# Optimization experiments

Hardware: AMD Instinct MI355X
Metric: run time of the kernel (lower is better)

The kernel has to match this reference:

```python
import jax, jax.numpy as jnp
import numpy as np


def setup_inputs() -> dict:
    key = jax.random.key(0)
    k1, = jax.random.split(key, 1)
    b, l, h, w, c = 2, 16, 16, 16, 32
    inputs = jax.random.normal(k1, (b, l, h, w, c), dtype=jnp.float32)
    gamma = jnp.ones((1,), dtype=jnp.float32)
    return {"inputs": inputs, "gamma": gamma}


def reference(inputs, gamma):
    b, l, h, w, c = inputs.shape
    n = l * h * w
    # torch: x = permute->view gives [b, c, n]; here keep [b, n, c] (same memory layout of values)
    xr = inputs.reshape(b, n, c)
    # scores[b,i,j] = sum_c x[b,c,i] * x[b,c,j]
    scores = jnp.einsum('bic,bjc->bij', xr, xr)
    attn = jax.nn.softmax(scores, axis=-1)  # softmax over j (dim=-1)
    # out[b,c,j] = sum_i x[b,c,i] * attn[b,i,j]  ->  [b, n, c] layout
    out = jnp.einsum('bic,bij->bjc', xr, attn)
    out = out.reshape(b, l, h, w, c)
    return out * gamma + inputs
```

## Files before the change

### kernel.cpp

```cpp
#include <hip/hip_runtime.h>


typedef _Float16 half8 __attribute__((ext_vector_type(8)));
typedef _Float16 half4v __attribute__((ext_vector_type(4)));
typedef float float4v __attribute__((ext_vector_type(4)));

#define NN 4096
#define CC 32
#define L2E 1.44269504f
#define SHIFT 48.0f

__global__ __launch_bounds__(256) void k_convert(const float* __restrict__ x,
                                                 _Float16* __restrict__ xf,
                                                 _Float16* __restrict__ xt) {
    const int t = blockIdx.x * 256 + threadIdx.x;
    const int n  = t & 4095;
    const int cg = (t >> 12) & 7;
    const int b  = t >> 15;
    const int row = (b << 12) | n;
    const float4* src = (const float4*)(x + (size_t)row * CC + cg * 4);
    float4 v = *src;
    _Float16 h0 = (_Float16)v.x, h1 = (_Float16)v.y, h2 = (_Float16)v.z, h3 = (_Float16)v.w;
    *(half4v*)(xf + (size_t)row * CC + cg * 4) = (half4v){h0, h1, h2, h3};
    _Float16* xtb = xt + (size_t)b * CC * NN;
    xtb[(cg * 4 + 0) * NN + n] = h0;
    xtb[(cg * 4 + 1) * NN + n] = h1;
    xtb[(cg * 4 + 2) * NN + n] = h2;
    xtb[(cg * 4 + 3) * NN + n] = h3;
}

__global__ __launch_bounds__(512) void k_pass1(const _Float16* __restrict__ xf,
                                               float* __restrict__ c2out) {
    const int tid = threadIdx.x;
    const int wave = tid >> 6, lane = tid & 63;
    const int quad = lane >> 4, l15 = lane & 15;
    const int b = blockIdx.x >> 8;
    const int i0 = (blockIdx.x & 255) * 16;
    const _Float16* xb = xf + (size_t)b * NN * CC;

    const half8 afrag = *(const half8*)(xb + (size_t)(i0 + l15) * CC + quad * 8);
    const float4v zf = {0.f, 0.f, 0.f, 0.f};
    float z[4] = {0.f, 0.f, 0.f, 0.f};
    const float c2c = -SHIFT * L2E;

    const int jbase = wave * 512;
    for (int jt = 0; jt < 8; ++jt) {
        const int j0 = jbase + jt * 64;
        half8 b0 = *(const half8*)(xb + (size_t)(j0 + l15) * CC + quad * 8);
        half8 b1 = *(const half8*)(xb + (size_t)(j0 + 16 + l15) * CC + quad * 8);
        half8 b2 = *(const half8*)(xb + (size_t)(j0 + 32 + l15) * CC + quad * 8);
        half8 b3 = *(const half8*)(xb + (size_t)(j0 + 48 + l15) * CC + quad * 8);
        float4v s0 = __builtin_amdgcn_mfma_f32_16x16x32_f16(afrag, b0, zf, 0, 0, 0);
        float4v s1 = __builtin_amdgcn_mfma_f32_16x16x32_f16(afrag, b1, zf, 0, 0, 0);
        float4v s2 = __builtin_amdgcn_mfma_f32_16x16x32_f16(afrag, b2, zf, 0, 0, 0);
        float4v s3 = __builtin_amdgcn_mfma_f32_16x16x32_f16(afrag, b3, zf, 0, 0, 0);
#pragma unroll
        for (int r = 0; r < 4; ++r) {
            z[r] += __builtin_amdgcn_exp2f(fmaf(s0[r], L2E, c2c));
            z[r] += __builtin_amdgcn_exp2f(fmaf(s1[r], L2E, c2c));
            z[r] += __builtin_amdgcn_exp2f(fmaf(s2[r], L2E, c2c));
            z[r] += __builtin_amdgcn_exp2f(fmaf(s3[r], L2E, c2c));
        }
    }
#pragma unroll
    for (int off = 1; off <= 8; off <<= 1) {
#pragma unroll
        for (int r = 0; r < 4; ++r) z[r] += __shfl_xor(z[r], off, 64);
    }
    __shared__ float zw[8][16];
    if (l15 == 0) {
#pragma unroll
        for (int r = 0; r < 4; ++r) zw[wave][quad * 4 + r] = z[r];
    }
    __syncthreads();
    if (tid < 16) {
        float zs = 0.f;
#pragma unroll
        for (int w = 0; w < 8; ++w) zs += zw[w][tid];
        c2out[b * NN + i0 + tid] = -(__builtin_amdgcn_logf(zs) + SHIFT * L2E);
    }
}

__global__ __launch_bounds__(512) void k_pass2(const _Float16* __restrict__ xf,
                                               const _Float16* __restrict__ xt,
                                               const float* __restrict__ c2,
                                               const float* __restrict__ x,
                                               const float* __restrict__ gamma,
                                               float* __restrict__ out) {
    const int tid = threadIdx.x;
    const int wave = tid >> 6, lane = tid & 63;
    const int quad = lane >> 4, l15 = lane & 15;
    const int b = blockIdx.x >> 8;
    const int j0 = (blockIdx.x & 255) * 16;
    const _Float16* xb  = xf + (size_t)b * NN * CC;
    const _Float16* xtb = xt + (size_t)b * CC * NN;
    const float* c2b = c2 + b * NN;

    __shared__ _Float16 pt[8][2][16 * 40];
    __shared__ float red[8][16][32];

    const half8 bjfrag = *(const half8*)(xb + (size_t)(j0 + l15) * CC + quad * 8);
    const float4v zf = {0.f, 0.f, 0.f, 0.f};
    float4v acc0 = zf, acc1 = zf;

    const int ibase = wave * 512;
    half8 a0  = *(const half8*)(xb + (size_t)(ibase + l15) * CC + quad * 8);
    half8 a1  = *(const half8*)(xb + (size_t)(ibase + 16 + l15) * CC + quad * 8);
    half8 xb0 = *(const half8*)(xtb + (size_t)l15 * NN + ibase + quad * 8);
    half8 xb1 = *(const half8*)(xtb + (size_t)(l15 + 16) * NN + ibase + quad * 8);
    float4v c20 = *(const float4v*)(c2b + ibase + quad * 4);
    float4v c21 = *(const float4v*)(c2b + ibase + 16 + quad * 4);

    for (int it = 0; it < 16; ++it) {
        const int inx = ibase + ((it + 1) & 15) * 32;
        half8 na0  = *(const half8*)(xb + (size_t)(inx + l15) * CC + quad * 8);
        half8 na1  = *(const half8*)(xb + (size_t)(inx + 16 + l15) * CC + quad * 8);
        half8 nxb0 = *(const half8*)(xtb + (size_t)l15 * NN + inx + quad * 8);
        half8 nxb1 = *(const half8*)(xtb + (size_t)(l15 + 16) * NN + inx + quad * 8);
        float4v nc20 = *(const float4v*)(c2b + inx + quad * 4);
        float4v nc21 = *(const float4v*)(c2b + inx + 16 + quad * 4);

        float4v s0 = __builtin_amdgcn_mfma_f32_16x16x32_f16(a0, bjfrag, zf, 0, 0, 0);
        float4v s1 = __builtin_amdgcn_mfma_f32_16x16x32_f16(a1, bjfrag, zf, 0, 0, 0);
        half4v p0, p1;
#pragma unroll
        for (int r = 0; r < 4; ++r) {
            p0[r] = (_Float16)__builtin_amdgcn_exp2f(fmaf(s0[r], L2E, c20[r]));
            p1[r] = (_Float16)__builtin_amdgcn_exp2f(fmaf(s1[r], L2E, c21[r]));
        }
        _Float16* ptw = &pt[wave][it & 1][0];
        *(half4v*)(ptw + l15 * 40 + quad * 4)      = p0;
        *(half4v*)(ptw + l15 * 40 + 16 + quad * 4) = p1;
        half8 a2 = *(const half8*)(ptw + l15 * 40 + quad * 8);
        acc0 = __builtin_amdgcn_mfma_f32_16x16x32_f16(a2, xb0, acc0, 0, 0, 0);
        acc1 = __builtin_amdgcn_mfma_f32_16x16x32_f16(a2, xb1, acc1, 0, 0, 0);

        a0 = na0; a1 = na1; xb0 = nxb0; xb1 = nxb1; c20 = nc20; c21 = nc21;
    }

#pragma unroll
    for (int r = 0; r < 4; ++r) {
        red[wave][quad * 4 + r][l15]      = acc0[r];
        red[wave][quad * 4 + r][l15 + 16] = acc1[r];
    }
    __syncthreads();
    {
        const int jj = tid >> 5, c = tid & 31;
        float s = 0.f;
#pragma unroll
        for (int w = 0; w < 8; ++w) s += red[w][jj][c];
        const float g = gamma[0];
        const size_t o = (size_t)(b * NN + j0 + jj) * CC + c;
        out[o] = fmaf(g, s, x[o]);
    }
}

extern "C" void kernel_launch(void* const* d_in, const int* in_sizes, int n_in,
                              void* d_out, int out_size, void* d_ws, size_t ws_size,
                              hipStream_t stream) {
    const float* x     = (const float*)d_in[0];
    const float* gamma = (const float*)d_in[1];
    float* out = (float*)d_out;

    _Float16* xf = (_Float16*)d_ws;
    _Float16* xt = xf + (size_t)2 * NN * CC;
    float*    c2 = (float*)(xt + (size_t)2 * CC * NN);

    k_convert<<<dim3(256), dim3(256), 0, stream>>>(x, xf, xt);
    k_pass1 <<<dim3(512), dim3(512), 0, stream>>>(xf, c2);
    k_pass2 <<<dim3(512), dim3(512), 0, stream>>>(xf, xt, c2, x, gamma, out);
}
```

Baseline: 94.69 us.

## Replace LDS P transpose with ds_bpermute, prefetch B in pass1, set occupancy hints

In pass2, the exp'd probabilities are packed to fp16 with cvt_pkrtz and rearranged into the MFMA A-operand layout using cross-lane ds_bpermute instead of a store/load round trip through shared memory. This drops the LDS staging buffer and its write/read latency. In exchange it issues eight bpermutes per iteration plus selects, and rounds toward zero instead of to nearest. Pass1 now software-prefetches the next B fragments, and both kernels gain a min-blocks-per-CU launch bound that can constrain register allocation.

```diff
diff --git a/kernel.cpp b/kernel.cpp
--- a/kernel.cpp
+++ b/kernel.cpp
@@ -3,7 +3,9 @@
 
 typedef _Float16 half8 __attribute__((ext_vector_type(8)));
 typedef _Float16 half4v __attribute__((ext_vector_type(4)));
+typedef _Float16 half2v __attribute__((ext_vector_type(2)));
 typedef float float4v __attribute__((ext_vector_type(4)));
+typedef int int4v __attribute__((ext_vector_type(4)));
 
 #define NN 4096
 #define CC 32
@@ -29,8 +31,8 @@
     xtb[(cg * 4 + 3) * NN + n] = h3;
 }
 
-__global__ __launch_bounds__(512) void k_pass1(const _Float16* __restrict__ xf,
-                                               float* __restrict__ c2out) {
+__global__ __launch_bounds__(512, 4) void k_pass1(const _Float16* __restrict__ xf,
+                                                  float* __restrict__ c2out) {
     const int tid = threadIdx.x;
     const int wave = tid >> 6, lane = tid & 63;
     const int quad = lane >> 4, l15 = lane & 15;
@@ -44,12 +46,18 @@
     const float c2c = -SHIFT * L2E;
 
     const int jbase = wave * 512;
+    half8 b0 = *(const half8*)(xb + (size_t)(jbase + l15) * CC + quad * 8);
+    half8 b1 = *(const half8*)(xb + (size_t)(jbase + 16 + l15) * CC + quad * 8);
+    half8 b2 = *(const half8*)(xb + (size_t)(jbase + 32 + l15) * CC + quad * 8);
+    half8 b3 = *(const half8*)(xb + (size_t)(jbase + 48 + l15) * CC + quad * 8);
+
     for (int jt = 0; jt < 8; ++jt) {
-        const int j0 = jbase + jt * 64;
-        half8 b0 = *(const half8*)(xb + (size_t)(j0 + l15) * CC + quad * 8);
-        half8 b1 = *(const half8*)(xb + (size_t)(j0 + 16 + l15) * CC + quad * 8);
-        half8 b2 = *(const half8*)(xb + (size_t)(j0 + 32 + l15) * CC + quad * 8);
-        half8 b3 = *(const half8*)(xb + (size_t)(j0 + 48 + l15) * CC + quad * 8);
+        const int jn = jbase + ((jt + 1) & 7) * 64;
+        half8 n0 = *(const half8*)(xb + (size_t)(jn + l15) * CC + quad * 8);
+        half8 n1 = *(const half8*)(xb + (size_t)(jn + 16 + l15) * CC + quad * 8);
+        half8 n2 = *(const half8*)(xb + (size_t)(jn + 32 + l15) * CC + quad * 8);
+        half8 n3 = *(const half8*)(xb + (size_t)(jn + 48 + l15) * CC + quad * 8);
+
         float4v s0 = __builtin_amdgcn_mfma_f32_16x16x32_f16(afrag, b0, zf, 0, 0, 0);
         float4v s1 = __builtin_amdgcn_mfma_f32_16x16x32_f16(afrag, b1, zf, 0, 0, 0);
         float4v s2 = __builtin_amdgcn_mfma_f32_16x16x32_f16(afrag, b2, zf, 0, 0, 0);
@@ -61,6 +69,7 @@
             z[r] += __builtin_amdgcn_exp2f(fmaf(s2[r], L2E, c2c));
             z[r] += __builtin_amdgcn_exp2f(fmaf(s3[r], L2E, c2c));
         }
+        b0 = n0; b1 = n1; b2 = n2; b3 = n3;
     }
 #pragma unroll
     for (int off = 1; off <= 8; off <<= 1) {
@@ -81,12 +90,12 @@
     }
 }
 
-__global__ __launch_bounds__(512) void k_pass2(const _Float16* __restrict__ xf,
-                                               const _Float16* __restrict__ xt,
-                                               const float* __restrict__ c2,
-                                               const float* __restrict__ x,
-                                               const float* __restrict__ gamma,
-                                               float* __restrict__ out) {
+__global__ __launch_bounds__(512, 4) void k_pass2(const _Float16* __restrict__ xf,
+                                                  const _Float16* __restrict__ xt,
+                                                  const float* __restrict__ c2,
+                                                  const float* __restrict__ x,
+                                                  const float* __restrict__ gamma,
+                                                  float* __restrict__ out) {
     const int tid = threadIdx.x;
     const int wave = tid >> 6, lane = tid & 63;
     const int quad = lane >> 4, l15 = lane & 15;
@@ -96,8 +105,11 @@
     const _Float16* xtb = xt + (size_t)b * CC * NN;
     const float* c2b = c2 + b * NN;
 
-    __shared__ _Float16 pt[8][2][16 * 40];
     __shared__ float red[8][16][32];
+
+    const int addrLo = (((quad & 1) << 5) + l15) << 2;
+    const int addrHi = addrLo + 64;
+    const bool lo32 = (lane < 32);
 
     const half8 bjfrag = *(const half8*)(xb + (size_t)(j0 + l15) * CC + quad * 8);
     const float4v zf = {0.f, 0.f, 0.f, 0.f};
@@ -122,16 +134,31 @@
 
         float4v s0 = __builtin_amdgcn_mfma_f32_16x16x32_f16(a0, bjfrag, zf, 0, 0, 0);
         float4v s1 = __builtin_amdgcn_mfma_f32_16x16x32_f16(a1, bjfrag, zf, 0, 0, 0);
-        half4v p0, p1;
+        float4v e0, e1;
 #pragma unroll
         for (int r = 0; r < 4; ++r) {
-            p0[r] = (_Float16)__builtin_amdgcn_exp2f(fmaf(s0[r], L2E, c20[r]));
-            p1[r] = (_Float16)__builtin_amdgcn_exp2f(fmaf(s1[r], L2E, c21[r]));
+            e0[r] = __builtin_amdgcn_exp2f(fmaf(s0[r], L2E, c20[r]));
+            e1[r] = __builtin_amdgcn_exp2f(fmaf(s1[r], L2E, c21[r]));
         }
-        _Float16* ptw = &pt[wave][it & 1][0];
-        *(half4v*)(ptw + l15 * 40 + quad * 4)      = p0;
-        *(half4v*)(ptw + l15 * 40 + 16 + quad * 4) = p1;
-        half8 a2 = *(const half8*)(ptw + l15 * 40 + quad * 8);
+        const int d0 = __builtin_bit_cast(int, (half2v)__builtin_amdgcn_cvt_pkrtz(e0[0], e0[1]));
+        const int d1 = __builtin_bit_cast(int, (half2v)__builtin_amdgcn_cvt_pkrtz(e0[2], e0[3]));
+        const int d2 = __builtin_bit_cast(int, (half2v)__builtin_amdgcn_cvt_pkrtz(e1[0], e1[1]));
+        const int d3 = __builtin_bit_cast(int, (half2v)__builtin_amdgcn_cvt_pkrtz(e1[2], e1[3]));
+        const int q0 = __builtin_amdgcn_ds_bpermute(addrLo, d0);
+        const int q1 = __builtin_amdgcn_ds_bpermute(addrLo, d1);
+        const int q2 = __builtin_amdgcn_ds_bpermute(addrHi, d0);
+        const int q3 = __builtin_amdgcn_ds_bpermute(addrHi, d1);
+        const int q4 = __builtin_amdgcn_ds_bpermute(addrLo, d2);
+        const int q5 = __builtin_amdgcn_ds_bpermute(addrLo, d3);
+        const int q6 = __builtin_amdgcn_ds_bpermute(addrHi, d2);
+        const int q7 = __builtin_amdgcn_ds_bpermute(addrHi, d3);
+        int4v ai;
+        ai[0] = lo32 ? q0 : q4;
+        ai[1] = lo32 ? q1 : q5;
+        ai[2] = lo32 ? q2 : q6;
+        ai[3] = lo32 ? q3 : q7;
+        const half8 a2 = __builtin_bit_cast(half8, ai);
+
         acc0 = __builtin_amdgcn_mfma_f32_16x16x32_f16(a2, xb0, acc0, 0, 0, 0);
         acc1 = __builtin_amdgcn_mfma_f32_16x16x32_f16(a2, xb1, acc1, 0, 0, 0);
 
```

After: 93.24 us. No clear change (-1.5%).
